# Kernel tuning notes

Measured on AMD Instinct MI355X. Metric: run time of the kernel, lower is better.

Reference implementation:

```python
import jax, jax.numpy as jnp
import numpy as np

B, T, Tc = 64, 256, 16
VW, VC, L = 100000, 128, 25
CE, CH = 25, 25          # char embed / char lstm hidden per direction
WE, WH = 100, 100        # word embed / word lstm hidden per direction (bi -> 200)
DW = WE + 2 * CH         # 150, word-LSTM input dim


def lstm(x, Wih, Whh, b):
    """Unidirectional LSTM over time axis 1. x: [N, S, D] -> [N, S, H]. PyTorch gate order i,f,g,o."""
    N = x.shape[0]
    H = Whh.shape[0]
    x_t = jnp.swapaxes(x, 0, 1)  # [S, N, D]

    def step(carry, xt):
        h, c = carry
        g = xt @ Wih + h @ Whh + b
        i, f, gg, o = jnp.split(g, 4, axis=-1)
        c = jax.nn.sigmoid(f) * c + jax.nn.sigmoid(i) * jnp.tanh(gg)
        h = jax.nn.sigmoid(o) * jnp.tanh(c)
        return (h, c), h

    h0 = jnp.zeros((N, H), x.dtype)
    _, hs = jax.lax.scan(step, (h0, h0), x_t)
    return jnp.swapaxes(hs, 0, 1)  # [N, S, H]


def crf_nll(em, tags, trans, start, end):
    """Negative log-likelihood of linear-chain CRF (no mask; full-length sequences)."""
    # gold path score
    em_score = jnp.take_along_axis(em, tags[:, :, None], axis=2).squeeze(-1).sum(axis=1)
    tr_score = trans[tags[:, :-1], tags[:, 1:]].sum(axis=1)
    gold = start[tags[:, 0]] + em_score + tr_score + end[tags[:, -1]]
    # forward algorithm (log partition)
    alpha0 = start[None, :] + em[:, 0]  # [B, L]

    def step(alpha, e_t):
        # alpha: [B, L] prev-tag scores; trans: [L, L]; e_t: [B, L]
        new = jax.nn.logsumexp(alpha[:, :, None] + trans[None, :, :] + e_t[:, None, :], axis=1)
        return new, None

    alpha, _ = jax.lax.scan(step, alpha0, jnp.swapaxes(em[:, 1:], 0, 1))
    logZ = jax.nn.logsumexp(alpha + end[None, :], axis=1)
    return jnp.sum(logZ - gold)


def setup_inputs():
    key = jax.random.key(0)
    ks = jax.random.split(key, 24)
    f = lambda i, shape: jax.random.normal(ks[i], shape, jnp.float32) * 0.1
    return {
        "tok_tensor": jax.random.randint(ks[0], (B, T), 0, VW),
        "tag_tensor": jax.random.randint(ks[1], (B, T), 0, L),
        "lengths": jnp.full((B,), T, jnp.int32),
        "char_tensor": jax.random.randint(ks[2], (B * T, Tc), 0, VC),
        "char_lengths": jax.random.randint(ks[3], (B * T,), 1, Tc + 1),
        "char_tensor_recover": jax.random.permutation(ks[4], B * T),
        "word_emb": f(5, (VW, WE)),
        "char_emb": f(6, (VC, CE)),
        "cWih_f": f(7, (CE, 4 * CH)), "cWhh_f": f(8, (CH, 4 * CH)), "cb_f": jnp.zeros((4 * CH,), jnp.float32),
        "cWih_b": f(9, (CE, 4 * CH)), "cWhh_b": f(10, (CH, 4 * CH)), "cb_b": jnp.zeros((4 * CH,), jnp.float32),
        "wWih_f": f(11, (DW, 4 * WH)), "wWhh_f": f(12, (WH, 4 * WH)), "wb_f": jnp.zeros((4 * WH,), jnp.float32),
        "wWih_b": f(13, (DW, 4 * WH)), "wWhh_b": f(14, (WH, 4 * WH)), "wb_b": jnp.zeros((4 * WH,), jnp.float32),
        "W_tag": f(15, (2 * WH, L)), "b_tag": jnp.zeros((L,), jnp.float32),
        "trans": f(16, (L, L)), "start": f(17, (L,)), "end": f(18, (L,)),
    }


def reference(tok_tensor, tag_tensor, lengths, char_tensor, char_lengths, char_tensor_recover,
              word_emb, char_emb,
              cWih_f, cWhh_f, cb_f, cWih_b, cWhh_b, cb_b,
              wWih_f, wWhh_f, wb_f, wWih_b, wWhh_b, wb_b,
              W_tag, b_tag, trans, start, end):
    N = char_tensor.shape[0]  # B*T words
    # ---- char BiLSTM: last hidden of each direction per word ----
    ce = char_emb[char_tensor]                      # [N, Tc, CE]
    last = char_lengths - 1
    hf = lstm(ce, cWih_f, cWhh_f, cb_f)             # [N, Tc, CH]
    h_fwd = hf[jnp.arange(N), last]                 # forward last valid hidden
    # backward: reverse each word within its length, scan, take hidden at step len-1
    t_ar = jnp.arange(Tc)[None, :]
    rev_idx = jnp.where(t_ar < char_lengths[:, None], char_lengths[:, None] - 1 - t_ar, t_ar)
    ce_rev = jnp.take_along_axis(ce, rev_idx[:, :, None], axis=1)
    hb = lstm(ce_rev, cWih_b, cWhh_b, cb_b)
    h_bwd = hb[jnp.arange(N), last]
    char_feat = jnp.concatenate([h_fwd, h_bwd], axis=-1)[char_tensor_recover].reshape(B, T, 2 * CH)
    # ---- concat word + char features (dropout = identity in eval) ----
    x = jnp.concatenate([word_emb[tok_tensor], char_feat], axis=-1)  # [B, T, DW]
    # ---- word BiLSTM (full-length sequences) ----
    h_f = lstm(x, wWih_f, wWhh_f, wb_f)
    h_b = jnp.flip(lstm(jnp.flip(x, axis=1), wWih_b, wWhh_b, wb_b), axis=1)
    seq = jnp.concatenate([h_f, h_b], axis=-1)       # [B, T, 2*WH]
    # ---- emissions + CRF NLL ----
    em = seq @ W_tag + b_tag                         # [B, T, L]
    return crf_nll(em, tag_tensor, trans, start, end)
```

## Files before the change

### kernel.cpp

```cpp
#include <hip/hip_runtime.h>
#include <hip/hip_bf16.h>

#define NB 64
#define NT 256
#define TC 16
#define NL 25
#define NWORDS 16384
#define DWd 150
#define WEd 100
#define WPB 5

__device__ __forceinline__ float sigf(float x){ return __fdividef(1.f, 1.f + __expf(-x)); }
__device__ __forceinline__ float tanhf_(float x){
    float ax = fabsf(x);
    float e = __expf(-2.f*ax);
    float r = (1.f - e) * __fdividef(1.f, 1.f + e);
    return copysignf(r, x);
}

__global__ void k_gxc(const float* __restrict__ char_emb,
                      const float* __restrict__ cWih_f, const float* __restrict__ cb_f,
                      const float* __restrict__ cWih_b, const float* __restrict__ cb_b,
                      float* __restrict__ gxc){
  int i = blockIdx.x*blockDim.x + threadIdx.x;
  if (i >= 128*2*100) return;
  int col = i % 100; int d = (i/100) & 1; int c = i/200;
  const float* Wih = d ? cWih_b : cWih_f;
  const float* bb  = d ? cb_b  : cb_f;
  float acc = bb[col];
  #pragma unroll
  for (int k=0;k<25;k++) acc += char_emb[c*25+k]*Wih[k*100+col];
  gxc[i] = acc;
}

__global__ __launch_bounds__(512) void k_char(const int* __restrict__ char_tensor,
   const int* __restrict__ char_lengths,
   const float* __restrict__ cWhh_f, const float* __restrict__ cWhh_b,
   const float* __restrict__ gxc, float* __restrict__ cf){
  __shared__ float h_lds[WPB][28];
  __shared__ float act[WPB][100];
  __shared__ int   chars[WPB][TC];
  __shared__ int   lens[WPB];
  int tid = threadIdx.x;
  int d  = blockIdx.x & 1;
  int wb = blockIdx.x >> 1;
  int w0 = wb*WPB;
  if (tid < WPB*TC){
    int ww = w0 + tid/TC;
    int cw = ww < NWORDS ? ww : NWORDS-1;
    chars[tid/TC][tid%TC] = char_tensor[cw*TC + (tid%TC)];
  }
  if (tid < WPB){
    int ww = w0 + tid;
    lens[tid] = char_lengths[ww < NWORDS ? ww : NWORDS-1];
  }
  int wsub = tid/100;
  int j    = tid - wsub*100;
  bool gate_thr = tid < WPB*100;
  const float* Wh = d ? cWhh_b : cWhh_f;
  float wcol[25];
  if (gate_thr){
    #pragma unroll
    for (int k=0;k<25;k++) wcol[k] = Wh[k*100 + j];
  }
  if (gate_thr && j < 28) h_lds[wsub][j] = 0.f;
  float c_reg = 0.f, h_last = 0.f;
  __syncthreads();
  int len = gate_thr ? lens[wsub] : 1;
  bool isg = (j >= 50) && (j < 75);
  float g_all[TC];
  if (gate_thr){
    #pragma unroll
    for (int t=0;t<TC;t++){
      int ci = d ? (len-1-t) : t;
      if (ci < 0 || ci >= TC) ci = 0;
      int cidx = chars[wsub][ci];
      g_all[t] = gxc[(size_t)(cidx*2+d)*100 + j];
    }
  }
  for (int t=0;t<TC;t++){
    if (gate_thr){
      float a = g_all[t];
      const float4* h4 = (const float4*)h_lds[wsub];
      #pragma unroll
      for (int kq=0;kq<6;kq++){
        float4 hq = h4[kq];
        a += hq.x*wcol[4*kq] + hq.y*wcol[4*kq+1] + hq.z*wcol[4*kq+2] + hq.w*wcol[4*kq+3];
      }
      a += h_lds[wsub][24]*wcol[24];
      act[wsub][j] = isg ? tanhf_(a) : sigf(a);
    }
    __syncthreads();
    if (gate_thr && j < 25 && t < len){
      float si = act[wsub][j], sf = act[wsub][25+j], sg = act[wsub][50+j], so = act[wsub][75+j];
      c_reg = sf*c_reg + si*sg;
      float hv = so*tanhf_(c_reg);
      h_lds[wsub][j] = hv;
      h_last = hv;
    }
    __syncthreads();
  }
  if (gate_thr && j < 25){
    int w = w0 + wsub;
    if (w < NWORDS) cf[(size_t)w*56 + d*28 + j] = h_last;
  }
}

__global__ __launch_bounds__(256) void k_wih(const int* __restrict__ tok,
    const int* __restrict__ recover,
    const float* __restrict__ word_emb, const float* __restrict__ cf,
    const float* __restrict__ Wf, const float* __restrict__ bf,
    const float* __restrict__ Wb, const float* __restrict__ bbias,
    float* __restrict__ gx){
  __shared__ float As[150][36];
  __shared__ int toks[32], recs[32];
  int tid = threadIdx.x;
  int m0 = (blockIdx.x>>2)*32;
  int nt = blockIdx.x & 3;
  int n0 = nt*256;
  if (tid < 32) toks[tid] = tok[m0 + tid];
  else if (tid < 64) recs[tid-32] = recover[m0 + tid - 32];
  __syncthreads();
  for (int i=tid; i<32*150; i+=256){
    int r = i/150; int k = i - r*150;
    float v;
    if (k < WEd) v = word_emb[(long)toks[r]*WEd + k];
    else {
      int ci = k - WEd;
      int dd = ci/25; int uu = ci - dd*25;
      v = cf[(size_t)recs[r]*56 + dd*28 + uu];
    }
    As[k][r] = v;
  }
  __syncthreads();
  int tn = tid & 31; int tm = tid >> 5;
  int j0 = n0 + tn*8;
  bool colok = j0 < 800;
  int d = (j0 >= 400) ? 1 : 0;
  const float* W = d ? Wb : Wf;
  int jc = j0 - d*400;
  float acc[4][8];
  #pragma unroll
  for (int mi=0;mi<4;mi++)
    #pragma unroll
    for (int ni=0;ni<8;ni++) acc[mi][ni]=0.f;
  if (colok){
    for (int k=0;k<150;k++){
      float4 b0 = *(const float4*)&W[k*400 + jc];
      float4 b1 = *(const float4*)&W[k*400 + jc + 4];
      float4 a4 = *(const float4*)&As[k][tm*4];
      float av[4] = {a4.x,a4.y,a4.z,a4.w};
      float bv[8] = {b0.x,b0.y,b0.z,b0.w,b1.x,b1.y,b1.z,b1.w};
      #pragma unroll
      for (int mi=0;mi<4;mi++)
        #pragma unroll
        for (int ni=0;ni<8;ni++) acc[mi][ni] += av[mi]*bv[ni];
    }
    const float* bptr = d ? bbias : bf;
    float bias[8];
    #pragma unroll
    for (int ni=0;ni<8;ni++) bias[ni] = bptr[jc+ni];
    #pragma unroll
    for (int mi=0;mi<4;mi++){
      int p = m0 + tm*4 + mi;
      float* orow = gx + ((long)d*NWORDS + p)*400 + jc;
      #pragma unroll
      for (int ni=0;ni<8;ni++) orow[ni] = acc[mi][ni] + bias[ni];
    }
  }
}

__global__ __launch_bounds__(448, 2) void k_wlstm(const float* __restrict__ gx,
     const float* __restrict__ Whf, const float* __restrict__ Whb,
     float* __restrict__ hseq){
  __shared__ float wstage[10000];
  __shared__ float h_lds[100];
  __shared__ float act[400];
  int tid = threadIdx.x;
  int s = blockIdx.x & 63; int d = blockIdx.x >> 6;
  const float* Wh = d ? Whb : Whf;
  int j = tid;
  bool colthr = j < 400;
  float wreg[100];
  #pragma unroll
  for (int ch=0; ch<4; ch++){
    for (int i=tid; i<2500; i+=448)
      ((float4*)wstage)[i] = ((const float4*)(Wh + ch*10000))[i];
    __syncthreads();
    if (colthr){
      #pragma unroll
      for (int kk=0;kk<25;kk++) wreg[ch*25+kk] = wstage[kk*400 + j];
    }
    __syncthreads();
  }
  if (tid < 100) h_lds[tid] = 0.f;
  float c_reg = 0.f;
  const float* gxd = gx + ((long)d*NWORDS + (long)s*256)*400;
  bool isg = (j >= 200) && (j < 300);
  __syncthreads();
  float gnext = 0.f;
  if (colthr) gnext = gxd[(d?255:0)*400 + j];
  for (int t=0;t<256;t++){
    float gcur = gnext;
    if (colthr && t+1 < 256){
      int tn = d ? (255-(t+1)) : (t+1);
      gnext = gxd[tn*400 + j];
    }
    if (colthr){
      float a = gcur;
      const float4* h4 = (const float4*)h_lds;
      #pragma unroll
      for (int kq=0;kq<25;kq++){
        float4 hq = h4[kq];
        a += hq.x*wreg[4*kq] + hq.y*wreg[4*kq+1] + hq.z*wreg[4*kq+2] + hq.w*wreg[4*kq+3];
      }
      act[j] = isg ? tanhf_(a) : sigf(a);
    }
    __syncthreads();
    if (tid < 100){
      float si = act[tid], sf = act[100+tid], sg = act[200+tid], so = act[300+tid];
      c_reg = sf*c_reg + si*sg;
      float hv = so*tanhf_(c_reg);
      h_lds[tid] = hv;
      int ttc = d ? (255-t) : t;
      hseq[((long)d*NWORDS + s*256 + ttc)*100 + tid] = hv;
    }
    __syncthreads();
  }
}

__global__ __launch_bounds__(256) void k_em(const float* __restrict__ hseq,
    const float* __restrict__ Wtag, const float* __restrict__ btag,
    float* __restrict__ em){
  __shared__ float hrow[8][200];
  __shared__ float Ws[5000];
  int tid = threadIdx.x;
  for (int i=tid;i<5000;i+=256) Ws[i] = Wtag[i];
  int p0 = blockIdx.x*8;
  for (int i=tid;i<8*200;i+=256){
    int r = i/200; int k = i - r*200;
    int p = p0+r;
    hrow[r][k] = (k<100) ? hseq[(long)p*100+k] : hseq[((long)NWORDS + p)*100 + (k-100)];
  }
  __syncthreads();
  int r = tid>>5; int c = tid&31;
  if (c<25){
    float acc = btag[c];
    for (int k=0;k<200;k++) acc += hrow[r][k]*Ws[k*25+c];
    em[(long)(p0+r)*25 + c] = acc;
  }
}

__global__ __launch_bounds__(64) void k_crf(const float* __restrict__ em,
    const int* __restrict__ tag, const float* __restrict__ trans,
    const float* __restrict__ start, const float* __restrict__ endv,
    float* __restrict__ part){
  int s = blockIdx.x;
  int lane = threadIdx.x;
  int j = lane & 31; int kg = lane >> 5;
  int k0 = kg ? 13 : 0; int kcnt = kg ? 12 : 13;
  const float* emb = em + (long)s*256*25;
  float tr[13];
  #pragma unroll
  for (int kk=0;kk<13;kk++){
    int k = k0+kk;
    tr[kk] = (k<25 && j<25) ? trans[k*25+j] : 0.f;
  }
  float alpha = (j<25) ? (start[j] + emb[j]) : -1e30f;
  float enext = (j<25) ? emb[25 + j] : 0.f;
  for (int t=1;t<256;t++){
    float ecur = enext;
    if (t<255 && j<25) enext = emb[(t+1)*25 + j];
    float m = -1e30f;
    #pragma unroll
    for (int kk=0;kk<13;kk++){
      if (kk<kcnt){
        float a = __shfl(alpha, k0+kk, 64);
        m = fmaxf(m, a + tr[kk]);
      }
    }
    m = fmaxf(m, __shfl_xor(m, 32, 64));
    float ssum = 0.f;
    #pragma unroll
    for (int kk=0;kk<13;kk++){
      if (kk<kcnt){
        float a = __shfl(alpha, k0+kk, 64);
        ssum += __expf(a + tr[kk] - m);
      }
    }
    ssum += __shfl_xor(ssum, 32, 64);
    float anew = __logf(ssum) + m + ecur;
    alpha = (j<25) ? anew : -1e30f;
  }
  float val = (j<25 && kg==0) ? (alpha + endv[j]) : -1e30f;
  float m2 = -1e30f;
  for (int k=0;k<25;k++) m2 = fmaxf(m2, __shfl(val, k, 64));
  float s2 = 0.f;
  for (int k=0;k<25;k++) s2 += __expf(__shfl(val, k, 64) - m2);
  float logZ = __logf(s2) + m2;
  const int* tg = tag + s*256;
  float gp = 0.f;
  for (int t=lane; t<256; t+=64){
    int a = tg[t];
    gp += emb[t*25 + a];
    if (t<255) gp += trans[a*25 + tg[t+1]];
  }
  #pragma unroll
  for (int off=32; off; off>>=1) gp += __shfl_xor(gp, off, 64);
  if (lane==0){
    float gold = gp + start[tg[0]] + endv[tg[255]];
    part[s] = logZ - gold;
  }
}

__global__ __launch_bounds__(64) void k_red(const float* __restrict__ part, float* __restrict__ out){
  float v = part[threadIdx.x];
  #pragma unroll
  for (int off=32; off; off>>=1) v += __shfl_xor(v, off, 64);
  if (threadIdx.x==0) out[0] = v;
}

extern "C" void kernel_launch(void* const* d_in, const int* in_sizes, int n_in,
                              void* d_out, int out_size, void* d_ws, size_t ws_size,
                              hipStream_t stream){
  const int* tok          = (const int*)d_in[0];
  const int* tagp         = (const int*)d_in[1];
  const int* char_tensor  = (const int*)d_in[3];
  const int* char_lengths = (const int*)d_in[4];
  const int* recover      = (const int*)d_in[5];
  const float* word_emb = (const float*)d_in[6];
  const float* char_emb = (const float*)d_in[7];
  const float* cWih_f=(const float*)d_in[8];  const float* cWhh_f=(const float*)d_in[9];  const float* cb_f=(const float*)d_in[10];
  const float* cWih_b=(const float*)d_in[11]; const float* cWhh_b=(const float*)d_in[12]; const float* cb_b=(const float*)d_in[13];
  const float* wWih_f=(const float*)d_in[14]; const float* wWhh_f=(const float*)d_in[15]; const float* wb_f=(const float*)d_in[16];
  const float* wWih_b=(const float*)d_in[17]; const float* wWhh_b=(const float*)d_in[18]; const float* wb_b=(const float*)d_in[19];
  const float* W_tag=(const float*)d_in[20];  const float* b_tag=(const float*)d_in[21];
  const float* trans=(const float*)d_in[22];  const float* startv=(const float*)d_in[23]; const float* endv=(const float*)d_in[24];

  float* ws  = (float*)d_ws;
  float* gxc = ws;
  float* cf  = ws + 25600;
  float* gx  = ws + 943104;
  float* hseq= ws + 14050304;
  float* em  = ws;
  float* part= ws + 17327104;
  float* out = (float*)d_out;

  k_gxc   <<<100, 256, 0, stream>>>(char_emb, cWih_f, cb_f, cWih_b, cb_b, gxc);
  k_char  <<<6554,512, 0, stream>>>(char_tensor, char_lengths, cWhh_f, cWhh_b, gxc, cf);
  k_wih   <<<2048,256, 0, stream>>>(tok, recover, word_emb, cf, wWih_f, wb_f, wWih_b, wb_b, gx);
  k_wlstm <<<128, 448, 0, stream>>>(gx, wWhh_f, wWhh_b, hseq);
  k_em    <<<2048,256, 0, stream>>>(hseq, W_tag, b_tag, em);
  k_crf   <<<64,  64,  0, stream>>>(em, tagp, trans, startv, endv, part);
  k_red   <<<1,   64,  0, stream>>>(part, out);
}
```

Baseline: 619.5 us.

## Prefetch char gates per step, enlarge GEMM row tile, simplify CRF with readlane

```diff
diff --git a/kernel.cpp b/kernel.cpp
--- a/kernel.cpp
+++ b/kernel.cpp
@@ -16,6 +16,9 @@
     float e = __expf(-2.f*ax);
     float r = (1.f - e) * __fdividef(1.f, 1.f + e);
     return copysignf(r, x);
+}
+__device__ __forceinline__ float RL(float v, int k){
+    return __int_as_float(__builtin_amdgcn_readlane(__float_as_int(v), k));
 }
 
 __global__ void k_gxc(const float* __restrict__ char_emb,
@@ -68,19 +71,21 @@
   __syncthreads();
   int len = gate_thr ? lens[wsub] : 1;
   bool isg = (j >= 50) && (j < 75);
-  float g_all[TC];
+  float gnext = 0.f;
   if (gate_thr){
-    #pragma unroll
-    for (int t=0;t<TC;t++){
-      int ci = d ? (len-1-t) : t;
+    int ci = d ? (len-1) : 0;
+    if (ci < 0 || ci >= TC) ci = 0;
+    gnext = gxc[(size_t)(chars[wsub][ci]*2+d)*100 + j];
+  }
+  for (int t=0;t<TC;t++){
+    float gcur = gnext;
+    if (gate_thr && t+1 < TC){
+      int ci = d ? (len-2-t) : (t+1);
       if (ci < 0 || ci >= TC) ci = 0;
-      int cidx = chars[wsub][ci];
-      g_all[t] = gxc[(size_t)(cidx*2+d)*100 + j];
-    }
-  }
-  for (int t=0;t<TC;t++){
+      gnext = gxc[(size_t)(chars[wsub][ci]*2+d)*100 + j];
+    }
     if (gate_thr){
-      float a = g_all[t];
+      float a = gcur;
       const float4* h4 = (const float4*)h_lds[wsub];
       #pragma unroll
       for (int kq=0;kq<6;kq++){
@@ -112,16 +117,16 @@
     const float* __restrict__ Wf, const float* __restrict__ bf,
     const float* __restrict__ Wb, const float* __restrict__ bbias,
     float* __restrict__ gx){
-  __shared__ float As[150][36];
-  __shared__ int toks[32], recs[32];
+  __shared__ float As[150][72];
+  __shared__ int toks[64], recs[64];
   int tid = threadIdx.x;
-  int m0 = (blockIdx.x>>2)*32;
+  int m0 = (blockIdx.x>>2)*64;
   int nt = blockIdx.x & 3;
   int n0 = nt*256;
-  if (tid < 32) toks[tid] = tok[m0 + tid];
-  else if (tid < 64) recs[tid-32] = recover[m0 + tid - 32];
-  __syncthreads();
-  for (int i=tid; i<32*150; i+=256){
+  if (tid < 64) toks[tid] = tok[m0 + tid];
+  else if (tid < 128) recs[tid-64] = recover[m0 + tid - 64];
+  __syncthreads();
+  for (int i=tid; i<64*150; i+=256){
     int r = i/150; int k = i - r*150;
     float v;
     if (k < WEd) v = word_emb[(long)toks[r]*WEd + k];
@@ -139,20 +144,21 @@
   int d = (j0 >= 400) ? 1 : 0;
   const float* W = d ? Wb : Wf;
   int jc = j0 - d*400;
-  float acc[4][8];
-  #pragma unroll
-  for (int mi=0;mi<4;mi++)
+  float acc[8][8];
+  #pragma unroll
+  for (int mi=0;mi<8;mi++)
     #pragma unroll
     for (int ni=0;ni<8;ni++) acc[mi][ni]=0.f;
   if (colok){
     for (int k=0;k<150;k++){
       float4 b0 = *(const float4*)&W[k*400 + jc];
       float4 b1 = *(const float4*)&W[k*400 + jc + 4];
-      float4 a4 = *(const float4*)&As[k][tm*4];
-      float av[4] = {a4.x,a4.y,a4.z,a4.w};
+      float4 a0 = *(const float4*)&As[k][tm*8];
+      float4 a1 = *(const float4*)&As[k][tm*8+4];
+      float av[8] = {a0.x,a0.y,a0.z,a0.w,a1.x,a1.y,a1.z,a1.w};
       float bv[8] = {b0.x,b0.y,b0.z,b0.w,b1.x,b1.y,b1.z,b1.w};
       #pragma unroll
-      for (int mi=0;mi<4;mi++)
+      for (int mi=0;mi<8;mi++)
         #pragma unroll
         for (int ni=0;ni<8;ni++) acc[mi][ni] += av[mi]*bv[ni];
     }
@@ -161,8 +167,8 @@
     #pragma unroll
     for (int ni=0;ni<8;ni++) bias[ni] = bptr[jc+ni];
     #pragma unroll
-    for (int mi=0;mi<4;mi++){
-      int p = m0 + tm*4 + mi;
+    for (int mi=0;mi<8;mi++){
+      int p = m0 + tm*8 + mi;
       float* orow = gx + ((long)d*NWORDS + p)*400 + jc;
       #pragma unroll
       for (int ni=0;ni<8;ni++) orow[ni] = acc[mi][ni] + bias[ni];
@@ -257,47 +263,38 @@
     float* __restrict__ part){
   int s = blockIdx.x;
   int lane = threadIdx.x;
-  int j = lane & 31; int kg = lane >> 5;
-  int k0 = kg ? 13 : 0; int kcnt = kg ? 12 : 13;
   const float* emb = em + (long)s*256*25;
-  float tr[13];
-  #pragma unroll
-  for (int kk=0;kk<13;kk++){
-    int k = k0+kk;
-    tr[kk] = (k<25 && j<25) ? trans[k*25+j] : 0.f;
-  }
-  float alpha = (j<25) ? (start[j] + emb[j]) : -1e30f;
-  float enext = (j<25) ? emb[25 + j] : 0.f;
+  float tr[25];
+  #pragma unroll
+  for (int k=0;k<25;k++) tr[k] = (lane<25) ? trans[k*25+lane] : 0.f;
+  float alpha = (lane<25) ? (start[lane] + emb[lane]) : 0.f;
+  float enext = (lane<25) ? emb[25+lane] : 0.f;
   for (int t=1;t<256;t++){
     float ecur = enext;
-    if (t<255 && j<25) enext = emb[(t+1)*25 + j];
-    float m = -1e30f;
-    #pragma unroll
-    for (int kk=0;kk<13;kk++){
-      if (kk<kcnt){
-        float a = __shfl(alpha, k0+kk, 64);
-        m = fmaxf(m, a + tr[kk]);
-      }
-    }
-    m = fmaxf(m, __shfl_xor(m, 32, 64));
-    float ssum = 0.f;
-    #pragma unroll
-    for (int kk=0;kk<13;kk++){
-      if (kk<kcnt){
-        float a = __shfl(alpha, k0+kk, 64);
-        ssum += __expf(a + tr[kk] - m);
-      }
-    }
-    ssum += __shfl_xor(ssum, 32, 64);
-    float anew = __logf(ssum) + m + ecur;
-    alpha = (j<25) ? anew : -1e30f;
-  }
-  float val = (j<25 && kg==0) ? (alpha + endv[j]) : -1e30f;
+    if (t<255 && lane<25) enext = emb[(t+1)*25 + lane];
+    float base = RL(alpha, 0);
+    float s0=0.f,s1=0.f,s2=0.f,s3=0.f,s4=0.f;
+    #pragma unroll
+    for (int k=0;k<5;k++) s0 += __expf(RL(alpha,k)    + tr[k]    - base);
+    #pragma unroll
+    for (int k=0;k<5;k++) s1 += __expf(RL(alpha,5+k)  + tr[5+k]  - base);
+    #pragma unroll
+    for (int k=0;k<5;k++) s2 += __expf(RL(alpha,10+k) + tr[10+k] - base);
+    #pragma unroll
+    for (int k=0;k<5;k++) s3 += __expf(RL(alpha,15+k) + tr[15+k] - base);
+    #pragma unroll
+    for (int k=0;k<5;k++) s4 += __expf(RL(alpha,20+k) + tr[20+k] - base);
+    float ssum = ((s0+s1)+(s2+s3))+s4;
+    alpha = __logf(ssum) + base + ecur;
+  }
+  float val = (lane<25) ? (alpha + endv[lane]) : -1e30f;
   float m2 = -1e30f;
-  for (int k=0;k<25;k++) m2 = fmaxf(m2, __shfl(val, k, 64));
-  float s2 = 0.f;
-  for (int k=0;k<25;k++) s2 += __expf(__shfl(val, k, 64) - m2);
-  float logZ = __logf(s2) + m2;
+  #pragma unroll
+  for (int k=0;k<25;k++) m2 = fmaxf(m2, RL(val,k));
+  float s2s = 0.f;
+  #pragma unroll
+  for (int k=0;k<25;k++) s2s += __expf(RL(val,k) - m2);
+  float logZ = __logf(s2s) + m2;
   const int* tg = tag + s*256;
   float gp = 0.f;
   for (int t=lane; t<256; t+=64){
@@ -348,7 +345,7 @@
 
   k_gxc   <<<100, 256, 0, stream>>>(char_emb, cWih_f, cb_f, cWih_b, cb_b, gxc);
   k_char  <<<6554,512, 0, stream>>>(char_tensor, char_lengths, cWhh_f, cWhh_b, gxc, cf);
-  k_wih   <<<2048,256, 0, stream>>>(tok, recover, word_emb, cf, wWih_f, wb_f, wWih_b, wb_b, gx);
+  k_wih   <<<1024,256, 0, stream>>>(tok, recover, word_emb, cf, wWih_f, wb_f, wWih_b, wb_b, gx);
   k_wlstm <<<128, 448, 0, stream>>>(gx, wWhh_f, wWhh_b, hseq);
   k_em    <<<2048,256, 0, stream>>>(hseq, W_tag, b_tag, em);
   k_crf   <<<64,  64,  0, stream>>>(em, tagp, trans, startv, endv, part);
```

Result: faster. 566.2 us (-8.6%).
